# Kernel optimization log

Measured on AMD Instinct MI355X. Metric: run time of the kernel, lower is better.

Reference implementation:

```python
import jax, jax.numpy as jnp
import numpy as np

L, B, T, D, H = 12, 8, 512, 768, 12
DH = D // H
EPS = 1e-12


def _layernorm(x, w, b):
    u = jnp.mean(x, axis=-1, keepdims=True)
    s = jnp.mean(jnp.square(x - u), axis=-1, keepdims=True)
    return w * ((x - u) / jnp.sqrt(s + EPS)) + b


def setup_inputs() -> dict:
    key = jax.random.key(0)
    ks = jax.random.split(key, 8)
    w = lambda k: jax.random.normal(k, (L, D, D), dtype=jnp.float32) * 0.02
    return {
        "query_states": jax.random.normal(ks[0], (B, T, D), dtype=jnp.float32),
        "hidden_states": jax.random.normal(ks[1], (B, T, D), dtype=jnp.float32),
        "attention_mask": jnp.zeros((B, 1, 1, T), dtype=jnp.float32),
        "Wq": w(ks[2]), "bq": jnp.zeros((L, D), jnp.float32),
        "Wk": w(ks[3]), "bk": jnp.zeros((L, D), jnp.float32),
        "Wv": w(ks[4]), "bv": jnp.zeros((L, D), jnp.float32),
        "Wo1": w(ks[5]), "bo1": jnp.zeros((L, D), jnp.float32),
        "ln1_w": jnp.ones((L, D), jnp.float32), "ln1_b": jnp.zeros((L, D), jnp.float32),
        "Wo2": w(ks[6]), "bo2": jnp.zeros((L, D), jnp.float32),
        "ln2_w": jnp.ones((L, D), jnp.float32), "ln2_b": jnp.zeros((L, D), jnp.float32),
    }


def reference(query_states, hidden_states, attention_mask,
              Wq, bq, Wk, bk, Wv, bv,
              Wo1, bo1, ln1_w, ln1_b,
              Wo2, bo2, ln2_w, ln2_b):
    scale = 1.0 / jnp.sqrt(jnp.float32(DH))

    def heads(x):  # [B,T,D] -> [B,H,T,DH]
        return x.reshape(B, T, H, DH).transpose(0, 2, 1, 3)

    def layer_fn(hidden, p):
        (wq, bq_, wk, bk_, wv, bv_, wo1, bo1_, l1w, l1b, wo2, bo2_, l2w, l2b) = p
        q = heads(query_states @ wq + bq_)
        k = heads(hidden @ wk + bk_)
        v = heads(hidden @ wv + bv_)
        scores = jnp.einsum("bhqd,bhkd->bhqk", q, k) * scale + attention_mask
        probs = jax.nn.softmax(scores, axis=-1)
        ctx = jnp.einsum("bhqk,bhkd->bhqd", probs, v)
        ctx = ctx.transpose(0, 2, 1, 3).reshape(B, T, D)
        # attention Output: LN(dense(ctx) + key_states)
        attn_out = _layernorm(ctx @ wo1 + bo1_ + hidden, l1w, l1b)
        # layer Output (intermediate is identity in source): LN(dense(attn_out) + attn_out)
        out = _layernorm(attn_out @ wo2 + bo2_ + attn_out, l2w, l2b)
        return out, None

    params = (Wq, bq, Wk, bk, Wv, bv, Wo1, bo1, ln1_w, ln1_b, Wo2, bo2, ln2_w, ln2_b)
    hidden, _ = jax.lax.scan(layer_fn, hidden_states, params)
    return hidden
```

## Files before the change

kernel.cpp:

```cpp
#include <hip/hip_runtime.h>
#include <stdint.h>

#define L_ 12
#define B_ 8
#define T_ 512
#define D_ 768
#define H_ 12
#define DH_ 64
#define M_ 4096
#define DD_ (D_*D_)

typedef unsigned short u16;
typedef __bf16 bf16x8 __attribute__((ext_vector_type(8)));
typedef float f32x4 __attribute__((ext_vector_type(4)));
typedef u16 u16x2 __attribute__((ext_vector_type(2)));
typedef u16 u16x4 __attribute__((ext_vector_type(4)));

static __device__ __forceinline__ u16 f2b(float f) {
  union { float f; unsigned u; } x; x.f = f;
  unsigned r = x.u + 0x7fffu + ((x.u >> 16) & 1u);
  return (u16)(r >> 16);
}
static __device__ __forceinline__ float b2f(u16 u) {
  union { unsigned u; float f; } x; x.u = ((unsigned)u) << 16; return x.f;
}
static __device__ __forceinline__ void gload16(u16* lds, const u16* g) {
  __builtin_amdgcn_global_load_lds((__attribute__((address_space(1))) void*)(g),
                                   (__attribute__((address_space(3))) void*)(lds), 16, 0, 0);
}
static __device__ __forceinline__ f32x4 mfma16(bf16x8 a, bf16x8 b, f32x4 c) {
  return __builtin_amdgcn_mfma_f32_16x16x32_bf16(a, b, c, 0, 0, 0);
}
static __device__ __forceinline__ bf16x8 ldfrag(const u16* p) {
  return *reinterpret_cast<const bf16x8*>(p);
}

__global__ void init_kernel(const float* __restrict__ qs, const float* __restrict__ hs,
                            u16* __restrict__ qsb, u16* __restrict__ hidb, int n) {
  int i = blockIdx.x * 256 + threadIdx.x;
  if (i < n) {
    qsb[i] = f2b(qs[i]);
    hidb[i] = f2b(hs[i]);
  }
}

__global__ void wt_kernel(const float* W0, const float* W1, const float* W2,
                          const float* W3, const float* W4, u16* __restrict__ out) {
  const int z = blockIdx.z, layer = z / 5, w = z % 5;
  const float* base = (w == 0) ? W0 : (w == 1) ? W1 : (w == 2) ? W2 : (w == 3) ? W3 : W4;
  const float* W = base + (size_t)layer * DD_;
  u16* O = out + (size_t)z * DD_;
  const int nb = blockIdx.x * 64, kb = blockIdx.y * 64;
  __shared__ u16 tile[64][66];
  const int tid = threadIdx.x;
  #pragma unroll
  for (int p = 0; p < 2; ++p) {
    const int idx = p * 256 + tid;
    const int rp = idx >> 4, n4 = (idx & 15) * 4;
    const f32x4 a = *reinterpret_cast<const f32x4*>(W + (size_t)(kb + 2 * rp) * D_ + nb + n4);
    const f32x4 b = *reinterpret_cast<const f32x4*>(W + (size_t)(kb + 2 * rp + 1) * D_ + nb + n4);
    #pragma unroll
    for (int i = 0; i < 4; i++) {
      u16x2 pr; pr[0] = f2b(a[i]); pr[1] = f2b(b[i]);
      *reinterpret_cast<u16x2*>(&tile[n4 + i][2 * rp]) = pr;
    }
  }
  __syncthreads();
  #pragma unroll
  for (int p = 0; p < 4; ++p) {
    const int idx = p * 256 + tid;
    const int n = idx >> 4, k4 = (idx & 15) * 4;
    u16x4 o4;
    #pragma unroll
    for (int i = 0; i < 4; i++) o4[i] = tile[n][k4 + i];
    *reinterpret_cast<u16x4*>(O + (size_t)(nb + n) * D_ + kb + k4) = o4;
  }
}

static __device__ void gemm_core(const u16* __restrict__ A, const u16* __restrict__ W,
                                 const float* __restrict__ bias, const u16* __restrict__ resb,
                                 float* __restrict__ outf, u16* __restrict__ outb,
                                 u16* __restrict__ outv) {
  __shared__ __align__(16) u16 lA[2][64 * 64];
  __shared__ __align__(16) u16 lB[2][128 * 64];
  const int tid = threadIdx.x;
  const int wave = tid >> 6, lane = tid & 63;
  const int wm = wave >> 1, wn = wave & 1;

  const int nbx = gridDim.x;
  const int nwg = nbx * gridDim.y;
  const int orig = blockIdx.y * nbx + blockIdx.x;
  const int cpx = nwg >> 3;
  const int swz = (orig & 7) * cpx + (orig >> 3);
  const int m0 = (swz / nbx) * 64, n0 = (swz % nbx) * 128;
  const int lr = lane & 15, lg = lane >> 4;

  f32x4 acc[2][4];
  #pragma unroll
  for (int i = 0; i < 2; i++)
    #pragma unroll
    for (int j = 0; j < 4; j++) acc[i][j] = f32x4{0.f, 0.f, 0.f, 0.f};

  const int uA0 = wave * 64 + lane, uA1 = 256 + uA0;
  const int rA0 = uA0 >> 3, cA0 = ((uA0 & 7) ^ (rA0 & 7)) << 3;
  const int rA1 = uA1 >> 3, cA1 = ((uA1 & 7) ^ (rA1 & 7)) << 3;
  const u16* Ab0 = A + (size_t)(m0 + rA0) * D_ + cA0;
  const u16* Ab1 = A + (size_t)(m0 + rA1) * D_ + cA1;
  const u16* Wb[4];
  #pragma unroll
  for (int q = 0; q < 4; ++q) {
    const int u = q * 256 + wave * 64 + lane;
    const int r = u >> 3, c = ((u & 7) ^ (r & 7)) << 3;
    Wb[q] = W + (size_t)(n0 + r) * D_ + c;
  }

#define STAGE(buf, k0_) do {                                   \
    gload16(lA[buf] + wave * 512,        Ab0 + (k0_));         \
    gload16(lA[buf] + 2048 + wave * 512, Ab1 + (k0_));         \
    gload16(lB[buf] + wave * 512,        Wb[0] + (k0_));       \
    gload16(lB[buf] + 2048 + wave * 512, Wb[1] + (k0_));       \
    gload16(lB[buf] + 4096 + wave * 512, Wb[2] + (k0_));       \
    gload16(lB[buf] + 6144 + wave * 512, Wb[3] + (k0_));       \
  } while (0)

  STAGE(0, 0);
  __syncthreads();

  const int sx = lr & 7;

  int cur = 0;
  for (int kt = 0; kt < 12; ++kt) {
    if (kt < 11) STAGE(cur ^ 1, (kt + 1) * 64);
    bf16x8 af[2][2], bw[2][4];
    #pragma unroll
    for (int kk = 0; kk < 2; ++kk) {
      const int uo = ((kk * 4 + lg) ^ sx) << 3;
      #pragma unroll
      for (int i = 0; i < 2; i++)
        af[kk][i] = ldfrag(lA[cur] + ((wm * 32 + i * 16 + lr) << 6) + uo);
      #pragma unroll
      for (int j = 0; j < 4; j++)
        bw[kk][j] = ldfrag(lB[cur] + ((wn * 64 + j * 16 + lr) << 6) + uo);
    }
    #pragma unroll
    for (int kk = 0; kk < 2; ++kk)
      #pragma unroll
      for (int i = 0; i < 2; i++)
        #pragma unroll
        for (int j = 0; j < 4; j++)
          acc[i][j] = mfma16(af[kk][i], bw[kk][j], acc[i][j]);
    __syncthreads();
    cur ^= 1;
  }
#undef STAGE

  if (outv) {
    #pragma unroll
    for (int j = 0; j < 4; j++) {
      const int colg = n0 + wn * 64 + j * 16 + lr;
      const float bv = bias[colg];
      const int h = colg >> 6, dh = colg & 63;
      #pragma unroll
      for (int i = 0; i < 2; i++) {
        const int rowb = m0 + wm * 32 + i * 16 + lg * 4;
        const int bb = rowb >> 9, t = rowb & 511;
        u16x4 o4;
        #pragma unroll
        for (int r = 0; r < 4; r++) o4[r] = f2b(acc[i][j][r] + bv);
        *reinterpret_cast<u16x4*>(outv + ((size_t)((bb * H_ + h) * DH_ + dh)) * T_ + t) = o4;
      }
    }
    return;
  }
  #pragma unroll
  for (int j = 0; j < 4; j++) {
    const int colg = n0 + wn * 64 + j * 16 + lr;
    const float bv = bias[colg];
    #pragma unroll
    for (int i = 0; i < 2; i++) {
      const int rowb = m0 + wm * 32 + i * 16 + lg * 4;
      #pragma unroll
      for (int r = 0; r < 4; r++) {
        float v = acc[i][j][r] + bv;
        const size_t off = (size_t)(rowb + r) * D_ + colg;
        if (resb) v += b2f(resb[off]);
        if (outf) outf[off] = v;
        if (outb) outb[off] = f2b(v);
      }
    }
  }
}

static __device__ void gemm128_core(const u16* __restrict__ A, const u16* __restrict__ W,
                                    const float* __restrict__ bias, u16* __restrict__ outb) {
  __shared__ __align__(16) u16 lA[2][128 * 64];
  __shared__ __align__(16) u16 lB[2][128 * 64];
  const int tid = threadIdx.x;
  const int wave = tid >> 6, lane = tid & 63;
  const int wm = wave >> 1, wn = wave & 1;

  const int nbx = gridDim.x;
  const int nwg = nbx * gridDim.y;
  const int orig = blockIdx.y * nbx + blockIdx.x;
  const int cpx = nwg >> 3;
  const int swz = (orig & 7) * cpx + (orig >> 3);
  const int m0 = (swz / nbx) * 128, n0 = (swz % nbx) * 128;
  const int lr = lane & 15, lg = lane >> 4;

  f32x4 acc[4][4];
  #pragma unroll
  for (int i = 0; i < 4; i++)
    #pragma unroll
    for (int j = 0; j < 4; j++) acc[i][j] = f32x4{0.f, 0.f, 0.f, 0.f};

  const u16* Ab[4];
  const u16* Wb[4];
  #pragma unroll
  for (int q = 0; q < 4; ++q) {
    const int u = q * 256 + wave * 64 + lane;
    const int r = u >> 3, c = ((u & 7) ^ (r & 7)) << 3;
    Ab[q] = A + (size_t)(m0 + r) * D_ + c;
    Wb[q] = W + (size_t)(n0 + r) * D_ + c;
  }

#define STAGE128(buf, k0_) do {                                \
    gload16(lA[buf] + wave * 512,        Ab[0] + (k0_));       \
    gload16(lA[buf] + 2048 + wave * 512, Ab[1] + (k0_));       \
    gload16(lA[buf] + 4096 + wave * 512, Ab[2] + (k0_));       \
    gload16(lA[buf] + 6144 + wave * 512, Ab[3] + (k0_));       \
    gload16(lB[buf] + wave * 512,        Wb[0] + (k0_));       \
    gload16(lB[buf] + 2048 + wave * 512, Wb[1] + (k0_));       \
    gload16(lB[buf] + 4096 + wave * 512, Wb[2] + (k0_));       \
    gload16(lB[buf] + 6144 + wave * 512, Wb[3] + (k0_));       \
  } while (0)

  STAGE128(0, 0);
  __syncthreads();

  const int sx = lr & 7;

  int cur = 0;
  for (int kt = 0; kt < 12; ++kt) {
    if (kt < 11) STAGE128(cur ^ 1, (kt + 1) * 64);
    #pragma unroll
    for (int kk = 0; kk < 2; ++kk) {
      const int uo = ((kk * 4 + lg) ^ sx) << 3;
      bf16x8 af[4], bw[4];
      #pragma unroll
      for (int i = 0; i < 4; i++)
        af[i] = ldfrag(lA[cur] + ((wm * 64 + i * 16 + lr) << 6) + uo);
      #pragma unroll
      for (int j = 0; j < 4; j++)
        bw[j] = ldfrag(lB[cur] + ((wn * 64 + j * 16 + lr) << 6) + uo);
      #pragma unroll
      for (int i = 0; i < 4; i++)
        #pragma unroll
        for (int j = 0; j < 4; j++)
          acc[i][j] = mfma16(af[i], bw[j], acc[i][j]);
    }
    __syncthreads();
    cur ^= 1;
  }
#undef STAGE128

  #pragma unroll
  for (int j = 0; j < 4; j++) {
    const int colg = n0 + wn * 64 + j * 16 + lr;
    const float bv = bias[colg];
    #pragma unroll
    for (int i = 0; i < 4; i++) {
      const int rowb = m0 + wm * 64 + i * 16 + lg * 4;
      #pragma unroll
      for (int r = 0; r < 4; r++)
        outb[(size_t)(rowb + r) * D_ + colg] = f2b(acc[i][j][r] + bv);
    }
  }
}

__global__ __launch_bounds__(256) void qall_kernel(const u16* qsb, const u16* wt60,
                                                   const float* bq, u16* qall) {
  const int l = blockIdx.z;
  gemm128_core(qsb, wt60 + (size_t)l * 5 * DD_, bq + l * D_, qall + (size_t)l * M_ * D_);
}

__global__ __launch_bounds__(256) void kv_kernel(const u16* hidb,
                                                 const u16* wk, const u16* wv,
                                                 const float* bk, const float* bv,
                                                 u16* kout, u16* vtout) {
  if (blockIdx.z == 0) gemm_core(hidb, wk, bk, nullptr, nullptr, kout, nullptr);
  else                 gemm_core(hidb, wv, bv, nullptr, nullptr, nullptr, vtout);
}

__global__ __launch_bounds__(256) void qkv3_kernel(const u16* qsb, const u16* hidb,
                                                   const u16* wq, const u16* wk, const u16* wv,
                                                   const float* bq, const float* bk, const float* bv,
                                                   u16* q, u16* kout, u16* vtout) {
  if (blockIdx.z == 0)      gemm_core(qsb,  wq, bq, nullptr, nullptr, q, nullptr);
  else if (blockIdx.z == 1) gemm_core(hidb, wk, bk, nullptr, nullptr, kout, nullptr);
  else                      gemm_core(hidb, wv, bv, nullptr, nullptr, nullptr, vtout);
}

__global__ __launch_bounds__(256) void o_kernel(const u16* A, const u16* W, const float* bias,
                                                const u16* resb, u16* yb) {
  gemm_core(A, W, bias, resb, nullptr, yb, nullptr);
}

__global__ __launch_bounds__(256) void attn_kernel(const u16* __restrict__ q, const u16* __restrict__ k,
                                                   const u16* __restrict__ vt, const float* __restrict__ mask,
                                                   u16* __restrict__ ctx) {
  __shared__ __align__(16) u16 KT[2][64 * 64];
  __shared__ __align__(16) u16 VT[2][64 * 64];
  __shared__ __align__(16) u16 PT[4 * 16 * 64];
  const int tid = threadIdx.x, wave = tid >> 6, lane = tid & 63;
  const int id = blockIdx.x;
  const int bh = id % 96, qblk = id / 96;
  const int b = bh / H_, h = bh % H_;
  const int q0 = qblk * 64 + wave * 16;
  const int lr = lane & 15, lg = lane >> 4;

  bf16x8 qa0, qa1;
  {
    const u16* qp = q + (size_t)(b * T_ + q0 + lr) * D_ + h * DH_ + lg * 8;
    qa0 = ldfrag(qp);
    qa1 = ldfrag(qp + 32);
  }

  const int su0 = wave * 64 + lane, su1 = 256 + wave * 64 + lane;
  const int sr0 = su0 >> 3, sc0 = ((su0 & 7) ^ (sr0 & 7)) << 3;
  const int sr1 = su1 >> 3, sc1 = ((su1 & 7) ^ (sr1 & 7)) << 3;
  const u16* kbase = k + (size_t)b * T_ * D_ + h * DH_;
  const u16* vbase = vt + (size_t)bh * DH_ * T_;

#define STAGEKV(buf, kt_) do {                                                         \
    gload16(KT[buf] + wave * 512,        kbase + (size_t)((kt_) * 64 + sr0) * D_ + sc0); \
    gload16(KT[buf] + 2048 + wave * 512, kbase + (size_t)((kt_) * 64 + sr1) * D_ + sc1); \
    gload16(VT[buf] + wave * 512,        vbase + (size_t)sr0 * T_ + (kt_) * 64 + sc0);   \
    gload16(VT[buf] + 2048 + wave * 512, vbase + (size_t)sr1 * T_ + (kt_) * 64 + sc1);   \
  } while (0)

  float mrow[4] = {-1e30f, -1e30f, -1e30f, -1e30f};
  float lrow[4] = {0.f, 0.f, 0.f, 0.f};
  f32x4 O[4] = { {0,0,0,0}, {0,0,0,0}, {0,0,0,0}, {0,0,0,0} };
  u16* Pw = PT + wave * 1024;

  STAGEKV(0, 0);
  int cur = 0;
  for (int kt = 0; kt < 8; ++kt) {
    __syncthreads();
    if (kt < 7) STAGEKV(cur ^ 1, kt + 1);

    f32x4 S[4];
    __builtin_amdgcn_s_setprio(1);
    #pragma unroll
    for (int nf = 0; nf < 4; ++nf) {
      const u16* kr = KT[cur] + (nf * 16 + lr) * 64;
      bf16x8 kb0 = ldfrag(kr + ((lg       ^ (lr & 7)) << 3));
      bf16x8 kb1 = ldfrag(kr + (((4 + lg) ^ (lr & 7)) << 3));
      f32x4 a = {0.f, 0.f, 0.f, 0.f};
      a = mfma16(qa0, kb0, a);
      a = mfma16(qa1, kb1, a);
      S[nf] = a;
    }
    __builtin_amdgcn_s_setprio(0);
    #pragma unroll
    for (int nf = 0; nf < 4; ++nf) {
      const float mk = mask[(size_t)b * T_ + kt * 64 + nf * 16 + lr];
      #pragma unroll
      for (int r = 0; r < 4; r++) S[nf][r] = S[nf][r] * 0.125f + mk;
    }
    #pragma unroll
    for (int r = 0; r < 4; r++) {
      float tm = fmaxf(fmaxf(S[0][r], S[1][r]), fmaxf(S[2][r], S[3][r]));
      #pragma unroll
      for (int d = 1; d <= 8; d <<= 1) tm = fmaxf(tm, __shfl_xor(tm, d));
      const float mn = fmaxf(mrow[r], tm);
      const float sc = __expf(mrow[r] - mn);
      float ts = 0.f;
      #pragma unroll
      for (int nf = 0; nf < 4; ++nf) { float pv = __expf(S[nf][r] - mn); S[nf][r] = pv; ts += pv; }
      #pragma unroll
      for (int d = 1; d <= 8; d <<= 1) ts += __shfl_xor(ts, d);
      lrow[r] = lrow[r] * sc + ts;
      mrow[r] = mn;
      #pragma unroll
      for (int nf = 0; nf < 4; ++nf) O[nf][r] *= sc;
    }
    #pragma unroll
    for (int nf = 0; nf < 4; ++nf)
      #pragma unroll
      for (int r = 0; r < 4; r++) {
        const int R = lg * 4 + r;
        Pw[R * 64 + ((((nf << 1) | (lr >> 3)) ^ (R & 7)) << 3) + (lr & 7)] = f2b(S[nf][r]);
      }
    __builtin_amdgcn_s_setprio(1);
    #pragma unroll
    for (int ks = 0; ks < 2; ++ks) {
      bf16x8 pa = ldfrag(Pw + lr * 64 + (((ks * 4 + lg) ^ (lr & 7)) << 3));
      #pragma unroll
      for (int nf = 0; nf < 4; ++nf) {
        bf16x8 vb = ldfrag(VT[cur] + (nf * 16 + lr) * 64 + (((ks * 4 + lg) ^ (lr & 7)) << 3));
        O[nf] = mfma16(pa, vb, O[nf]);
      }
    }
    __builtin_amdgcn_s_setprio(0);
    cur ^= 1;
  }
#undef STAGEKV

  #pragma unroll
  for (int r = 0; r < 4; r++) {
    const float inv = 1.f / lrow[r];
    const int row = q0 + lg * 4 + r;
    #pragma unroll
    for (int nf = 0; nf < 4; ++nf)
      ctx[(size_t)(b * T_ + row) * D_ + h * DH_ + nf * 16 + lr] = f2b(O[nf][r] * inv);
  }
}

__global__ __launch_bounds__(256) void ln_kernel(const u16* __restrict__ y,
                                                 const float* __restrict__ w, const float* __restrict__ bp,
                                                 float* __restrict__ outf, u16* __restrict__ outb) {
  const int wave = threadIdx.x >> 6, lane = threadIdx.x & 63;
  const int row = blockIdx.x * 4 + wave;
  const u16x4* yp = (const u16x4*)(y + (size_t)row * D_);
  f32x4 x[3];
  #pragma unroll
  for (int j = 0; j < 3; j++) {
    const u16x4 r4 = yp[j * 64 + lane];
    #pragma unroll
    for (int c = 0; c < 4; c++) x[j][c] = b2f(r4[c]);
  }
  float s = 0.f;
  #pragma unroll
  for (int j = 0; j < 3; j++) s += x[j][0] + x[j][1] + x[j][2] + x[j][3];
  #pragma unroll
  for (int d = 1; d <= 32; d <<= 1) s += __shfl_xor(s, d);
  const float u = s * (1.f / D_);
  float v = 0.f;
  #pragma unroll
  for (int j = 0; j < 3; j++)
    #pragma unroll
    for (int c = 0; c < 4; c++) { float t = x[j][c] - u; v += t * t; }
  #pragma unroll
  for (int d = 1; d <= 32; d <<= 1) v += __shfl_xor(v, d);
  const float rinv = rsqrtf(v * (1.f / D_) + 1e-12f);
  const f32x4* wp = (const f32x4*)w;
  const f32x4* bpp = (const f32x4*)bp;
  #pragma unroll
  for (int j = 0; j < 3; j++) {
    const f32x4 w4 = wp[j * 64 + lane];
    const f32x4 b4 = bpp[j * 64 + lane];
    f32x4 o4;
    u16x4 ob;
    #pragma unroll
    for (int c = 0; c < 4; c++) {
      o4[c] = w4[c] * ((x[j][c] - u) * rinv) + b4[c];
      ob[c] = f2b(o4[c]);
    }
    if (outf) ((f32x4*)(outf + (size_t)row * D_))[j * 64 + lane] = o4;
    ((u16x4*)(outb + (size_t)row * D_))[j * 64 + lane] = ob;
  }
}

extern "C" void kernel_launch(void* const* d_in, const int* in_sizes, int n_in,
                              void* d_out, int out_size, void* d_ws, size_t ws_size,
                              hipStream_t stream) {
  const float* qs   = (const float*)d_in[0];
  const float* hs   = (const float*)d_in[1];
  const float* mask = (const float*)d_in[2];
  const float* Wq   = (const float*)d_in[3];
  const float* bq   = (const float*)d_in[4];
  const float* Wk   = (const float*)d_in[5];
  const float* bk   = (const float*)d_in[6];
  const float* Wv   = (const float*)d_in[7];
  const float* bv   = (const float*)d_in[8];
  const float* Wo1  = (const float*)d_in[9];
  const float* bo1  = (const float*)d_in[10];
  const float* l1w  = (const float*)d_in[11];
  const float* l1b  = (const float*)d_in[12];
  const float* Wo2  = (const float*)d_in[13];
  const float* bo2  = (const float*)d_in[14];
  const float* l2w  = (const float*)d_in[15];
  const float* l2b  = (const float*)d_in[16];
  float* out = (float*)d_out;

  char* p = (char*)d_ws;
  auto alloc = [&](size_t bytes) { char* r = p; p += (bytes + 255) & ~(size_t)255; return r; };
  u16*   qsb  = (u16*)alloc((size_t)M_ * D_ * 2);
  u16*   hidb = (u16*)alloc((size_t)M_ * D_ * 2);
  u16*   kb_  = (u16*)alloc((size_t)M_ * D_ * 2);
  u16*   vtb  = (u16*)alloc((size_t)M_ * D_ * 2);
  u16*   ctxb = (u16*)alloc((size_t)M_ * D_ * 2);
  u16*   yb   = (u16*)alloc((size_t)M_ * D_ * 2);
  u16*   aob  = (u16*)alloc((size_t)M_ * D_ * 2);
  u16*   qb   = (u16*)alloc((size_t)M_ * D_ * 2);
  const size_t base_used = (size_t)(p - (char*)d_ws);
  const size_t wt60_bytes = (size_t)60 * DD_ * 2;
  const size_t qall_bytes = (size_t)12 * M_ * D_ * 2;
  const bool wt_once  = (ws_size - base_used) >= wt60_bytes + 512;
  u16* wt60 = (u16*)alloc(wt_once ? wt60_bytes : (size_t)5 * DD_ * 2);
  const size_t used2 = (size_t)(p - (char*)d_ws);
  const bool q_all   = wt_once && (ws_size - used2) >= qall_bytes + 512;
  u16* qall = q_all ? (u16*)alloc(qall_bytes) : qb;

  init_kernel<<<(M_ * D_ + 255) / 256, 256, 0, stream>>>(qs, hs, qsb, hidb, M_ * D_);
  if (wt_once)
    wt_kernel<<<dim3(12, 12, 60), 256, 0, stream>>>(Wq, Wk, Wv, Wo1, Wo2, wt60);
  if (q_all)
    qall_kernel<<<dim3(6, 32, 12), 256, 0, stream>>>(qsb, wt60, bq, qall);

  for (int l = 0; l < L_; ++l) {
    const size_t wo = (size_t)l * DD_;
    u16* wt = wt_once ? (wt60 + (size_t)l * 5 * DD_) : wt60;
    if (!wt_once)
      wt_kernel<<<dim3(12, 12, 5), 256, 0, stream>>>(Wq + wo, Wk + wo, Wv + wo, Wo1 + wo, Wo2 + wo, wt);
    const u16* qcur;
    if (q_all) {
      qcur = qall + (size_t)l * M_ * D_;
      kv_kernel<<<dim3(6, 64, 2), 256, 0, stream>>>(hidb, wt + DD_, wt + 2 * DD_,
                                                    bk + l * D_, bv + l * D_, kb_, vtb);
    } else {
      qcur = qb;
      qkv3_kernel<<<dim3(6, 64, 3), 256, 0, stream>>>(qsb, hidb,
          wt, wt + DD_, wt + 2 * DD_, bq + l * D_, bk + l * D_, bv + l * D_, qb, kb_, vtb);
    }
    attn_kernel<<<768, 256, 0, stream>>>(qcur, kb_, vtb, mask, ctxb);
    o_kernel<<<dim3(6, 64), 256, 0, stream>>>(ctxb, wt + 3 * DD_, bo1 + l * D_, hidb, yb);
    ln_kernel<<<1024, 256, 0, stream>>>(yb, l1w + l * D_, l1b + l * D_, nullptr, aob);
    o_kernel<<<dim3(6, 64), 256, 0, stream>>>(aob, wt + 4 * DD_, bo2 + l * D_, aob, yb);
    ln_kernel<<<1024, 256, 0, stream>>>(yb, l2w + l * D_, l2b + l * D_,
                                        (l == L_ - 1) ? out : nullptr, hidb);
  }
}
```

Measured before the change: 1.115 ms.

## Process 32 query rows per wave in attention to reuse K/V tiles

Each wave in the attention kernel now handles two 16-row query groups instead of one, so every block covers 128 query rows and the grid shrinks from 768 to 384 blocks. Each K and V fragment loaded from shared memory feeds two MFMAs, which halves global K/V staging traffic per query row. The cost is roughly double the accumulator and softmax registers, which may lower occupancy, and fewer blocks (384) on a large GPU, which may leave compute units underused.

```diff
diff --git a/kernel.cpp b/kernel.cpp
--- a/kernel.cpp
+++ b/kernel.cpp
@@ -310,19 +310,20 @@
                                                    u16* __restrict__ ctx) {
   __shared__ __align__(16) u16 KT[2][64 * 64];
   __shared__ __align__(16) u16 VT[2][64 * 64];
-  __shared__ __align__(16) u16 PT[4 * 16 * 64];
+  __shared__ __align__(16) u16 PT[4 * 32 * 64];
   const int tid = threadIdx.x, wave = tid >> 6, lane = tid & 63;
   const int id = blockIdx.x;
   const int bh = id % 96, qblk = id / 96;
   const int b = bh / H_, h = bh % H_;
-  const int q0 = qblk * 64 + wave * 16;
+  const int q0 = qblk * 128 + wave * 32;
   const int lr = lane & 15, lg = lane >> 4;
 
-  bf16x8 qa0, qa1;
-  {
-    const u16* qp = q + (size_t)(b * T_ + q0 + lr) * D_ + h * DH_ + lg * 8;
-    qa0 = ldfrag(qp);
-    qa1 = ldfrag(qp + 32);
+  bf16x8 qa[2][2];
+  #pragma unroll
+  for (int rg = 0; rg < 2; ++rg) {
+    const u16* qp = q + (size_t)(b * T_ + q0 + rg * 16 + lr) * D_ + h * DH_ + lg * 8;
+    qa[rg][0] = ldfrag(qp);
+    qa[rg][1] = ldfrag(qp + 32);
   }
 
   const int su0 = wave * 64 + lane, su1 = 256 + wave * 64 + lane;
@@ -338,10 +339,16 @@
     gload16(VT[buf] + 2048 + wave * 512, vbase + (size_t)sr1 * T_ + (kt_) * 64 + sc1);   \
   } while (0)
 
-  float mrow[4] = {-1e30f, -1e30f, -1e30f, -1e30f};
-  float lrow[4] = {0.f, 0.f, 0.f, 0.f};
-  f32x4 O[4] = { {0,0,0,0}, {0,0,0,0}, {0,0,0,0}, {0,0,0,0} };
-  u16* Pw = PT + wave * 1024;
+  float mrow[2][4], lrow[2][4];
+  f32x4 O[2][4];
+  #pragma unroll
+  for (int rg = 0; rg < 2; ++rg)
+    #pragma unroll
+    for (int r = 0; r < 4; r++) {
+      mrow[rg][r] = -1e30f; lrow[rg][r] = 0.f;
+      O[rg][r] = f32x4{0.f, 0.f, 0.f, 0.f};
+    }
+  u16* Pw = PT + wave * 2048;
 
   STAGEKV(0, 0);
   int cur = 0;
@@ -349,57 +356,71 @@
     __syncthreads();
     if (kt < 7) STAGEKV(cur ^ 1, kt + 1);
 
-    f32x4 S[4];
+    f32x4 S[2][4];
     __builtin_amdgcn_s_setprio(1);
     #pragma unroll
     for (int nf = 0; nf < 4; ++nf) {
       const u16* kr = KT[cur] + (nf * 16 + lr) * 64;
       bf16x8 kb0 = ldfrag(kr + ((lg       ^ (lr & 7)) << 3));
       bf16x8 kb1 = ldfrag(kr + (((4 + lg) ^ (lr & 7)) << 3));
-      f32x4 a = {0.f, 0.f, 0.f, 0.f};
-      a = mfma16(qa0, kb0, a);
-      a = mfma16(qa1, kb1, a);
-      S[nf] = a;
+      #pragma unroll
+      for (int rg = 0; rg < 2; ++rg) {
+        f32x4 a = {0.f, 0.f, 0.f, 0.f};
+        a = mfma16(qa[rg][0], kb0, a);
+        a = mfma16(qa[rg][1], kb1, a);
+        S[rg][nf] = a;
+      }
     }
     __builtin_amdgcn_s_setprio(0);
     #pragma unroll
     for (int nf = 0; nf < 4; ++nf) {
       const float mk = mask[(size_t)b * T_ + kt * 64 + nf * 16 + lr];
       #pragma unroll
-      for (int r = 0; r < 4; r++) S[nf][r] = S[nf][r] * 0.125f + mk;
-    }
-    #pragma unroll
-    for (int r = 0; r < 4; r++) {
-      float tm = fmaxf(fmaxf(S[0][r], S[1][r]), fmaxf(S[2][r], S[3][r]));
-      #pragma unroll
-      for (int d = 1; d <= 8; d <<= 1) tm = fmaxf(tm, __shfl_xor(tm, d));
-      const float mn = fmaxf(mrow[r], tm);
-      const float sc = __expf(mrow[r] - mn);
-      float ts = 0.f;
-      #pragma unroll
-      for (int nf = 0; nf < 4; ++nf) { float pv = __expf(S[nf][r] - mn); S[nf][r] = pv; ts += pv; }
-      #pragma unroll
-      for (int d = 1; d <= 8; d <<= 1) ts += __shfl_xor(ts, d);
-      lrow[r] = lrow[r] * sc + ts;
-      mrow[r] = mn;
-      #pragma unroll
-      for (int nf = 0; nf < 4; ++nf) O[nf][r] *= sc;
-    }
-    #pragma unroll
-    for (int nf = 0; nf < 4; ++nf)
+      for (int rg = 0; rg < 2; ++rg)
+        #pragma unroll
+        for (int r = 0; r < 4; r++) S[rg][nf][r] = S[rg][nf][r] * 0.125f + mk;
+    }
+    #pragma unroll
+    for (int rg = 0; rg < 2; ++rg)
       #pragma unroll
       for (int r = 0; r < 4; r++) {
-        const int R = lg * 4 + r;
-        Pw[R * 64 + ((((nf << 1) | (lr >> 3)) ^ (R & 7)) << 3) + (lr & 7)] = f2b(S[nf][r]);
+        float tm = fmaxf(fmaxf(S[rg][0][r], S[rg][1][r]), fmaxf(S[rg][2][r], S[rg][3][r]));
+        #pragma unroll
+        for (int d = 1; d <= 8; d <<= 1) tm = fmaxf(tm, __shfl_xor(tm, d));
+        const float mn = fmaxf(mrow[rg][r], tm);
+        const float sc = __expf(mrow[rg][r] - mn);
+        float ts = 0.f;
+        #pragma unroll
+        for (int nf = 0; nf < 4; ++nf) { float pv = __expf(S[rg][nf][r] - mn); S[rg][nf][r] = pv; ts += pv; }
+        #pragma unroll
+        for (int d = 1; d <= 8; d <<= 1) ts += __shfl_xor(ts, d);
+        lrow[rg][r] = lrow[rg][r] * sc + ts;
+        mrow[rg][r] = mn;
+        #pragma unroll
+        for (int nf = 0; nf < 4; ++nf) O[rg][nf][r] *= sc;
       }
+    #pragma unroll
+    for (int rg = 0; rg < 2; ++rg)
+      #pragma unroll
+      for (int nf = 0; nf < 4; ++nf)
+        #pragma unroll
+        for (int r = 0; r < 4; r++) {
+          const int R = rg * 16 + lg * 4 + r;
+          Pw[R * 64 + ((((nf << 1) | (lr >> 3)) ^ (R & 7)) << 3) + (lr & 7)] = f2b(S[rg][nf][r]);
+        }
     __builtin_amdgcn_s_setprio(1);
     #pragma unroll
     for (int ks = 0; ks < 2; ++ks) {
-      bf16x8 pa = ldfrag(Pw + lr * 64 + (((ks * 4 + lg) ^ (lr & 7)) << 3));
+      bf16x8 pa[2];
+      #pragma unroll
+      for (int rg = 0; rg < 2; ++rg)
+        pa[rg] = ldfrag(Pw + (rg * 16 + lr) * 64 + (((ks * 4 + lg) ^ (lr & 7)) << 3));
       #pragma unroll
       for (int nf = 0; nf < 4; ++nf) {
         bf16x8 vb = ldfrag(VT[cur] + (nf * 16 + lr) * 64 + (((ks * 4 + lg) ^ (lr & 7)) << 3));
-        O[nf] = mfma16(pa, vb, O[nf]);
+        #pragma unroll
+        for (int rg = 0; rg < 2; ++rg)
+          O[rg][nf] = mfma16(pa[rg], vb, O[rg][nf]);
       }
     }
     __builtin_amdgcn_s_setprio(0);
@@ -408,13 +429,15 @@
 #undef STAGEKV
 
   #pragma unroll
-  for (int r = 0; r < 4; r++) {
-    const float inv = 1.f / lrow[r];
-    const int row = q0 + lg * 4 + r;
-    #pragma unroll
-    for (int nf = 0; nf < 4; ++nf)
-      ctx[(size_t)(b * T_ + row) * D_ + h * DH_ + nf * 16 + lr] = f2b(O[nf][r] * inv);
-  }
+  for (int rg = 0; rg < 2; ++rg)
+    #pragma unroll
+    for (int r = 0; r < 4; r++) {
+      const float inv = 1.f / lrow[rg][r];
+      const int row = q0 + rg * 16 + lg * 4 + r;
+      #pragma unroll
+      for (int nf = 0; nf < 4; ++nf)
+        ctx[(size_t)(b * T_ + row) * D_ + h * DH_ + nf * 16 + lr] = f2b(O[rg][nf][r] * inv);
+    }
 }
 
 __global__ __launch_bounds__(256) void ln_kernel(const u16* __restrict__ y,
@@ -524,7 +547,7 @@
       qkv3_kernel<<<dim3(6, 64, 3), 256, 0, stream>>>(qsb, hidb,
           wt, wt + DD_, wt + 2 * DD_, bq + l * D_, bk + l * D_, bv + l * D_, qb, kb_, vtb);
     }
-    attn_kernel<<<768, 256, 0, stream>>>(qcur, kb_, vtb, mask, ctxb);
+    attn_kernel<<<384, 256, 0, stream>>>(qcur, kb_, vtb, mask, ctxb);
     o_kernel<<<dim3(6, 64), 256, 0, stream>>>(ctxb, wt + 3 * DD_, bo1 + l * D_, hidb, yb);
     ln_kernel<<<1024, 256, 0, stream>>>(yb, l1w + l * D_, l1b + l * D_, nullptr, aob);
     o_kernel<<<dim3(6, 64), 256, 0, stream>>>(aob, wt + 4 * DD_, bo2 + l * D_, aob, yb);
```

Result: slower. 1.184 ms (+6.2%).

## Use 32-row GEMM tiles for output projections and restructure weight transpose

Applied to the files above, without the earlier changes.

Adds a gemm32_core with 32x128 tiles in which each wave owns a 32-column slice, and uses it for both output-projection GEMMs. This doubles the workgroup count (768 instead of 384) so more CUs stay busy on the 4096x768x768 GEMMs. The weight-transpose kernel now processes 32 full columns per block with wider vector stores, and the final layer no longer writes the unused bf16 hidden copy. The cost is less operand reuse per tile and more redundant loads of the weight tiles.

```diff
diff --git a/kernel.cpp b/kernel.cpp
--- a/kernel.cpp
+++ b/kernel.cpp
@@ -13,7 +13,6 @@
 typedef unsigned short u16;
 typedef __bf16 bf16x8 __attribute__((ext_vector_type(8)));
 typedef float f32x4 __attribute__((ext_vector_type(4)));
-typedef u16 u16x2 __attribute__((ext_vector_type(2)));
 typedef u16 u16x4 __attribute__((ext_vector_type(4)));
 
 static __device__ __forceinline__ u16 f2b(float f) {
@@ -46,34 +45,36 @@
 
 __global__ void wt_kernel(const float* W0, const float* W1, const float* W2,
                           const float* W3, const float* W4, u16* __restrict__ out) {
-  const int z = blockIdx.z, layer = z / 5, w = z % 5;
+  const int z = blockIdx.y, layer = z / 5, w = z % 5;
   const float* base = (w == 0) ? W0 : (w == 1) ? W1 : (w == 2) ? W2 : (w == 3) ? W3 : W4;
   const float* W = base + (size_t)layer * DD_;
   u16* O = out + (size_t)z * DD_;
-  const int nb = blockIdx.x * 64, kb = blockIdx.y * 64;
-  __shared__ u16 tile[64][66];
-  const int tid = threadIdx.x;
-  #pragma unroll
-  for (int p = 0; p < 2; ++p) {
-    const int idx = p * 256 + tid;
-    const int rp = idx >> 4, n4 = (idx & 15) * 4;
-    const f32x4 a = *reinterpret_cast<const f32x4*>(W + (size_t)(kb + 2 * rp) * D_ + nb + n4);
-    const f32x4 b = *reinterpret_cast<const f32x4*>(W + (size_t)(kb + 2 * rp + 1) * D_ + nb + n4);
+  const int nb = blockIdx.x * 32;
+  __shared__ u16 tile[32][772];
+  const int t = threadIdx.x;
+  #pragma unroll
+  for (int p = 0; p < 6; ++p) {
+    const int g = p * 256 + t;
+    const int n4 = (g & 7) * 4, kr4 = (g >> 3) * 4;
+    f32x4 v[4];
+    #pragma unroll
+    for (int j = 0; j < 4; j++)
+      v[j] = *reinterpret_cast<const f32x4*>(W + (size_t)(kr4 + j) * D_ + nb + n4);
     #pragma unroll
     for (int i = 0; i < 4; i++) {
-      u16x2 pr; pr[0] = f2b(a[i]); pr[1] = f2b(b[i]);
-      *reinterpret_cast<u16x2*>(&tile[n4 + i][2 * rp]) = pr;
+      u16x4 w4;
+      #pragma unroll
+      for (int j = 0; j < 4; j++) w4[j] = f2b(v[j][i]);
+      *reinterpret_cast<u16x4*>(&tile[n4 + i][kr4]) = w4;
     }
   }
   __syncthreads();
   #pragma unroll
-  for (int p = 0; p < 4; ++p) {
-    const int idx = p * 256 + tid;
-    const int n = idx >> 4, k4 = (idx & 15) * 4;
-    u16x4 o4;
-    #pragma unroll
-    for (int i = 0; i < 4; i++) o4[i] = tile[n][k4 + i];
-    *reinterpret_cast<u16x4*>(O + (size_t)(nb + n) * D_ + kb + k4) = o4;
+  for (int p = 0; p < 24; ++p) {
+    const int q = p * 256 + t;
+    const int n = q / 192, k4 = (q - n * 192) * 4;
+    const u16x4 o4 = *reinterpret_cast<const u16x4*>(&tile[n][k4]);
+    *reinterpret_cast<u16x4*>(O + (size_t)(nb + n) * D_ + k4) = o4;
   }
 }
 
@@ -163,11 +164,11 @@
       #pragma unroll
       for (int i = 0; i < 2; i++) {
         const int rowb = m0 + wm * 32 + i * 16 + lg * 4;
-        const int bb = rowb >> 9, t = rowb & 511;
+        const int bb = rowb >> 9, tt = rowb & 511;
         u16x4 o4;
         #pragma unroll
         for (int r = 0; r < 4; r++) o4[r] = f2b(acc[i][j][r] + bv);
-        *reinterpret_cast<u16x4*>(outv + ((size_t)((bb * H_ + h) * DH_ + dh)) * T_ + t) = o4;
+        *reinterpret_cast<u16x4*>(outv + ((size_t)((bb * H_ + h) * DH_ + dh)) * T_ + tt) = o4;
       }
     }
     return;
@@ -186,6 +187,96 @@
         if (resb) v += b2f(resb[off]);
         if (outf) outf[off] = v;
         if (outb) outb[off] = f2b(v);
+      }
+    }
+  }
+}
+
+static __device__ void gemm32_core(const u16* __restrict__ A, const u16* __restrict__ W,
+                                   const float* __restrict__ bias, const u16* __restrict__ resb,
+                                   u16* __restrict__ outb) {
+  __shared__ __align__(16) u16 lA[2][32 * 64];
+  __shared__ __align__(16) u16 lB[2][128 * 64];
+  const int tid = threadIdx.x;
+  const int wave = tid >> 6, lane = tid & 63;
+
+  const int nbx = gridDim.x;
+  const int nwg = nbx * gridDim.y;
+  const int orig = blockIdx.y * nbx + blockIdx.x;
+  const int cpx = nwg >> 3;
+  const int swz = (orig & 7) * cpx + (orig >> 3);
+  const int m0 = (swz / nbx) * 32, n0 = (swz % nbx) * 128;
+  const int lr = lane & 15, lg = lane >> 4;
+
+  f32x4 acc[2][2];
+  #pragma unroll
+  for (int i = 0; i < 2; i++)
+    #pragma unroll
+    for (int j = 0; j < 2; j++) acc[i][j] = f32x4{0.f, 0.f, 0.f, 0.f};
+
+  const int uA = wave * 64 + lane;
+  const int rA = uA >> 3, cA = ((uA & 7) ^ (rA & 7)) << 3;
+  const u16* Ab = A + (size_t)(m0 + rA) * D_ + cA;
+  const u16* Wb[4];
+  #pragma unroll
+  for (int q = 0; q < 4; ++q) {
+    const int u = q * 256 + wave * 64 + lane;
+    const int r = u >> 3, c = ((u & 7) ^ (r & 7)) << 3;
+    Wb[q] = W + (size_t)(n0 + r) * D_ + c;
+  }
+
+#define STAGE32(buf, k0_) do {                                 \
+    gload16(lA[buf] + wave * 512,        Ab + (k0_));          \
+    gload16(lB[buf] + wave * 512,        Wb[0] + (k0_));       \
+    gload16(lB[buf] + 2048 + wave * 512, Wb[1] + (k0_));       \
+    gload16(lB[buf] + 4096 + wave * 512, Wb[2] + (k0_));       \
+    gload16(lB[buf] + 6144 + wave * 512, Wb[3] + (k0_));       \
+  } while (0)
+
+  STAGE32(0, 0);
+  __syncthreads();
+
+  const int sx = lr & 7;
+
+  int cur = 0;
+  for (int kt = 0; kt < 12; ++kt) {
+    if (kt < 11) STAGE32(cur ^ 1, (kt + 1) * 64);
+    bf16x8 af[2][2], bw[2][2];
+    #pragma unroll
+    for (int kk = 0; kk < 2; ++kk) {
+      const int uo = ((kk * 4 + lg) ^ sx) << 3;
+      #pragma unroll
+      for (int i = 0; i < 2; i++)
+        af[kk][i] = ldfrag(lA[cur] + ((i * 16 + lr) << 6) + uo);
+      #pragma unroll
+      for (int j = 0; j < 2; j++)
+        bw[kk][j] = ldfrag(lB[cur] + ((wave * 32 + j * 16 + lr) << 6) + uo);
+    }
+    #pragma unroll
+    for (int kk = 0; kk < 2; ++kk)
+      #pragma unroll
+      for (int i = 0; i < 2; i++)
+        #pragma unroll
+        for (int j = 0; j < 2; j++)
+          acc[i][j] = mfma16(af[kk][i], bw[kk][j], acc[i][j]);
+    __syncthreads();
+    cur ^= 1;
+  }
+#undef STAGE32
+
+  #pragma unroll
+  for (int j = 0; j < 2; j++) {
+    const int colg = n0 + wave * 32 + j * 16 + lr;
+    const float bv = bias[colg];
+    #pragma unroll
+    for (int i = 0; i < 2; i++) {
+      const int rowb = m0 + i * 16 + lg * 4;
+      #pragma unroll
+      for (int r = 0; r < 4; r++) {
+        float v = acc[i][j][r] + bv;
+        const size_t off = (size_t)(rowb + r) * D_ + colg;
+        if (resb) v += b2f(resb[off]);
+        outb[off] = f2b(v);
       }
     }
   }
@@ -302,7 +393,7 @@
 
 __global__ __launch_bounds__(256) void o_kernel(const u16* A, const u16* W, const float* bias,
                                                 const u16* resb, u16* yb) {
-  gemm_core(A, W, bias, resb, nullptr, yb, nullptr);
+  gemm32_core(A, W, bias, resb, yb);
 }
 
 __global__ __launch_bounds__(256) void attn_kernel(const u16* __restrict__ q, const u16* __restrict__ k,
@@ -458,7 +549,7 @@
       ob[c] = f2b(o4[c]);
     }
     if (outf) ((f32x4*)(outf + (size_t)row * D_))[j * 64 + lane] = o4;
-    ((u16x4*)(outb + (size_t)row * D_))[j * 64 + lane] = ob;
+    if (outb) ((u16x4*)(outb + (size_t)row * D_))[j * 64 + lane] = ob;
   }
 }
 
@@ -505,7 +596,7 @@
 
   init_kernel<<<(M_ * D_ + 255) / 256, 256, 0, stream>>>(qs, hs, qsb, hidb, M_ * D_);
   if (wt_once)
-    wt_kernel<<<dim3(12, 12, 60), 256, 0, stream>>>(Wq, Wk, Wv, Wo1, Wo2, wt60);
+    wt_kernel<<<dim3(24, 60), 256, 0, stream>>>(Wq, Wk, Wv, Wo1, Wo2, wt60);
   if (q_all)
     qall_kernel<<<dim3(6, 32, 12), 256, 0, stream>>>(qsb, wt60, bq, qall);
 
@@ -513,7 +604,7 @@
     const size_t wo = (size_t)l * DD_;
     u16* wt = wt_once ? (wt60 + (size_t)l * 5 * DD_) : wt60;
     if (!wt_once)
-      wt_kernel<<<dim3(12, 12, 5), 256, 0, stream>>>(Wq + wo, Wk + wo, Wv + wo, Wo1 + wo, Wo2 + wo, wt);
+      wt_kernel<<<dim3(24, 5), 256, 0, stream>>>(Wq + wo, Wk + wo, Wv + wo, Wo1 + wo, Wo2 + wo, wt);
     const u16* qcur;
     if (q_all) {
       qcur = qall + (size_t)l * M_ * D_;
@@ -525,10 +616,11 @@
           wt, wt + DD_, wt + 2 * DD_, bq + l * D_, bk + l * D_, bv + l * D_, qb, kb_, vtb);
     }
     attn_kernel<<<768, 256, 0, stream>>>(qcur, kb_, vtb, mask, ctxb);
-    o_kernel<<<dim3(6, 64), 256, 0, stream>>>(ctxb, wt + 3 * DD_, bo1 + l * D_, hidb, yb);
+    o_kernel<<<dim3(6, 128), 256, 0, stream>>>(ctxb, wt + 3 * DD_, bo1 + l * D_, hidb, yb);
     ln_kernel<<<1024, 256, 0, stream>>>(yb, l1w + l * D_, l1b + l * D_, nullptr, aob);
-    o_kernel<<<dim3(6, 64), 256, 0, stream>>>(aob, wt + 4 * DD_, bo2 + l * D_, aob, yb);
+    o_kernel<<<dim3(6, 128), 256, 0, stream>>>(aob, wt + 4 * DD_, bo2 + l * D_, aob, yb);
     ln_kernel<<<1024, 256, 0, stream>>>(yb, l2w + l * D_, l2b + l * D_,
-                                        (l == L_ - 1) ? out : nullptr, hidb);
-  }
-}
+                                        (l == L_ - 1) ? out : nullptr,
+                                        (l == L_ - 1) ? nullptr : hidb);
+  }
+}
```

Measured after the change: 1.152 ms. 3.3% more time.
